# Kernel optimization log

Hardware: AMD Instinct MI355X
Metric: run time of the kernel (lower is better)

Reference implementation:

```python
import jax, jax.numpy as jnp
import numpy as np

N_NODES = 100000
N_EDGES = 1600000
IN_DIM, HID_DIM, OUT_DIM = 128, 64, 1


def setup_inputs() -> dict:
    key = jax.random.key(0)
    ks = jax.random.split(key, 8)
    x = jax.random.normal(ks[0], (N_NODES, IN_DIM), dtype=jnp.float32)
    edge_index = jax.random.randint(ks[1], (2, N_EDGES), 0, N_NODES, dtype=jnp.int64)
    # Glorot-ish scaled weights
    W1 = jax.random.normal(ks[2], (IN_DIM, HID_DIM), dtype=jnp.float32) / np.sqrt(IN_DIM)
    b1 = jnp.zeros((HID_DIM,), dtype=jnp.float32)
    W2 = jax.random.normal(ks[3], (HID_DIM, HID_DIM), dtype=jnp.float32) / np.sqrt(HID_DIM)
    b2 = jnp.zeros((HID_DIM,), dtype=jnp.float32)
    W3 = jax.random.normal(ks[4], (HID_DIM, OUT_DIM), dtype=jnp.float32) / np.sqrt(HID_DIM)
    b3 = jnp.zeros((OUT_DIM,), dtype=jnp.float32)
    return {"x": x, "edge_index": edge_index, "W1": W1, "b1": b1,
            "W2": W2, "b2": b2, "W3": W3, "b3": b3}


def _gcn_norm(edge_index, num_nodes):
    # PyG gcn_norm with add_self_loops=True, edge_weight=1:
    # deg[i] = 1 (self loop) + #incoming edges at i (dst = edge_index[1])
    dst = edge_index[1]
    deg = jnp.ones((num_nodes,), dtype=jnp.float32).at[dst].add(1.0)
    dis = jnp.where(deg > 0, 1.0 / jnp.sqrt(deg), 0.0)  # deg_inv_sqrt
    return dis


def _gcn_conv(x, W, b, src, dst, dis):
    h = x @ W                                   # [N, F_out] transform first (PyG order)
    norm = dis[src] * dis[dst]                  # [E]
    msg = h[src] * norm[:, None]                # gather + scale, [E, F_out]
    out = jnp.zeros_like(h).at[dst].add(msg)    # scatter-add aggregation
    out = out + h * (dis * dis)[:, None]        # self-loop contribution
    return out + b


def reference(x, edge_index, W1, b1, W2, b2, W3, b3):
    src, dst = edge_index[0], edge_index[1]
    dis = _gcn_norm(edge_index, x.shape[0])
    h = jax.nn.relu(_gcn_conv(x, W1, b1, src, dst, dis))   # dropout = identity (eval)
    h = jax.nn.relu(_gcn_conv(h, W2, b2, src, dst, dis))
    return _gcn_conv(h, W3, b3, src, dst, dis)
```

## Files before the change

### kernel.cpp

```cpp
#include <hip/hip_runtime.h>

#define IN_DIM 128
#define HID 64
#define MAXC 400
#define MAXB 512
#define EPB 4096
#define DPT 512
#define G1CAP 6144

static __device__ __forceinline__ unsigned short f2bf(float f) {
    unsigned u = __float_as_uint(f);
    u += 0x7FFF + ((u >> 16) & 1);
    return (unsigned short)(u >> 16);
}

typedef short bf16x8 __attribute__((ext_vector_type(8)));
typedef float f32x4 __attribute__((ext_vector_type(4)));

__global__ __launch_bounds__(256) void k_hist2(const int* __restrict__ dst,
                                               int* __restrict__ hmat, int E, int NC) {
    __shared__ int h[MAXC];
    int tid = threadIdx.x, blk = blockIdx.x;
    for (int i = tid; i < NC; i += 256) h[i] = 0;
    __syncthreads();
    int e0 = blk * EPB, e1 = min(e0 + EPB, E);
    for (int e = e0 + tid; e < e1; e += 256) atomicAdd(&h[dst[e] >> 8], 1);
    __syncthreads();
    for (int i = tid; i < NC; i += 256) hmat[blk * MAXC + i] = h[i];
}

__global__ __launch_bounds__(512) void k_bktscan(int* __restrict__ hmat,
                                                 int* __restrict__ bktTotal,
                                                 int NBLK, int NC) {
    __shared__ int tmp[512];
    int cb = blockIdx.x;
    int t = threadIdx.x;
    int v = (t < NBLK) ? hmat[t * MAXC + cb] : 0;
    tmp[t] = v;
    __syncthreads();
    for (int off = 1; off < 512; off <<= 1) {
        int a = (t >= off) ? tmp[t - off] : 0;
        __syncthreads();
        tmp[t] += a;
        __syncthreads();
    }
    if (t < NBLK) hmat[t * MAXC + cb] = tmp[t] - v;
    if (t == 511) bktTotal[cb] = tmp[511];
}

__global__ __launch_bounds__(512) void k_cscan(const int* __restrict__ bktTotal,
                                               int* __restrict__ coarseStart,
                                               int* __restrict__ rowStart,
                                               int NC, int N, int E) {
    __shared__ int tmp[512];
    int t = threadIdx.x;
    int v = (t < NC) ? bktTotal[t] : 0;
    tmp[t] = v;
    __syncthreads();
    for (int off = 1; off < 512; off <<= 1) {
        int a = (t >= off) ? tmp[t - off] : 0;
        __syncthreads();
        tmp[t] += a;
        __syncthreads();
    }
    int excl = tmp[t] - v;
    if (t < NC) coarseStart[t] = excl;
    if (t == NC - 1) coarseStart[NC] = excl + v;
    if (t == 0) rowStart[N] = E;
}

__global__ __launch_bounds__(256) void k_part1(const int* __restrict__ src,
                                               const int* __restrict__ dst,
                                               const int* __restrict__ hmat,
                                               const int* __restrict__ coarseStart,
                                               int* __restrict__ tmp1,
                                               int E, int NC) {
    __shared__ int bcnt[MAXC];
    __shared__ int bbase[MAXC];
    int tid = threadIdx.x, blk = blockIdx.x;
    for (int i = tid; i < NC; i += 256) {
        bcnt[i] = 0;
        bbase[i] = coarseStart[i] + hmat[blk * MAXC + i];
    }
    __syncthreads();
    int e0 = blk * EPB, e1 = min(e0 + EPB, E);
    for (int e = e0 + tid; e < e1; e += 256) {
        int s = src[e], d = dst[e];
        int cb = d >> 8;
        int slot = bbase[cb] + atomicAdd(&bcnt[cb], 1);
        tmp1[slot] = s | ((d & 255) << 17);
    }
}

__global__ __launch_bounds__(DPT) void k_degplace(const int* __restrict__ tmp1,
                                                  const int* __restrict__ coarseStart,
                                                  float* __restrict__ dis,
                                                  int* __restrict__ rowStart,
                                                  int* __restrict__ esrc, int N) {
    __shared__ int hist[256];
    __shared__ int scn[256];
    __shared__ int cur[256];
    int tid = threadIdx.x;
    int cb = blockIdx.x;
    int node0 = cb << 8;
    const int r0 = coarseStart[cb], r1 = coarseStart[cb + 1];
    if (tid < 256) hist[tid] = 0;
    __syncthreads();
    for (int i = r0 + tid; i < r1; i += DPT)
        atomicAdd(&hist[((unsigned)tmp1[i]) >> 17], 1);
    __syncthreads();
    int v = 0;
    if (tid < 256) { v = hist[tid]; scn[tid] = v; }
    __syncthreads();
    for (int off = 1; off < 256; off <<= 1) {
        int a = 0;
        if (tid < 256 && tid >= off) a = scn[tid - off];
        __syncthreads();
        if (tid < 256) scn[tid] += a;
        __syncthreads();
    }
    if (tid < 256) {
        int myStart = r0 + scn[tid] - v;
        cur[tid] = myStart;
        int node = node0 + tid;
        if (node < N) {
            dis[node] = rsqrtf((float)v + 1.0f);
            rowStart[node] = myStart;
        }
    }
    __syncthreads();
    for (int i = r0 + tid; i < r1; i += DPT) {
        int pk = tmp1[i];
        int dl = ((unsigned)pk) >> 17;
        int pos = atomicAdd(&cur[dl], 1);
        esrc[pos] = (pk & 0x1FFFF) << 7;
    }
}

template <int K, typename T>
__global__ __launch_bounds__(256) void k_mmx(const T* __restrict__ X,
                                             const float* __restrict__ W,
                                             const float* __restrict__ dis,
                                             unsigned short* __restrict__ Hbs, int N) {
    constexpr int WP = K + 8;
    __shared__ unsigned short Wt[64 * WP];
    const int tid = threadIdx.x;
    for (int i = tid; i < K * 64; i += 256) {
        int k = i >> 6, n = i & 63;
        Wt[n * WP + k] = f2bf(W[i]);
    }
    __syncthreads();
    const int lane = tid & 63;
    const int m16 = lane & 15;
    const int quad = lane >> 4;
    const int rowBase = blockIdx.x * 64 + (tid >> 6) * 16;
    const int rowc = min(rowBase + m16, N - 1);

    f32x4 acc0 = {0.f, 0.f, 0.f, 0.f};
    f32x4 acc1 = acc0, acc2 = acc0, acc3 = acc0;
    const T* xrow = X + (size_t)rowc * K;
#pragma unroll
    for (int k0 = 0; k0 < K; k0 += 32) {
        bf16x8 af;
        if constexpr (sizeof(T) == 4) {
            const float* xp = (const float*)xrow + k0 + quad * 8;
            float4 xa = *(const float4*)xp;
            float4 xb = *(const float4*)(xp + 4);
            af[0] = (short)f2bf(xa.x); af[1] = (short)f2bf(xa.y);
            af[2] = (short)f2bf(xa.z); af[3] = (short)f2bf(xa.w);
            af[4] = (short)f2bf(xb.x); af[5] = (short)f2bf(xb.y);
            af[6] = (short)f2bf(xb.z); af[7] = (short)f2bf(xb.w);
        } else {
            af = *(const bf16x8*)((const unsigned short*)xrow + k0 + quad * 8);
        }
        const unsigned short* wp = &Wt[m16 * WP + k0 + quad * 8];
        bf16x8 b0 = *(const bf16x8*)(wp);
        bf16x8 b1 = *(const bf16x8*)(wp + 16 * WP);
        bf16x8 b2 = *(const bf16x8*)(wp + 32 * WP);
        bf16x8 b3 = *(const bf16x8*)(wp + 48 * WP);
        acc0 = __builtin_amdgcn_mfma_f32_16x16x32_bf16(af, b0, acc0, 0, 0, 0);
        acc1 = __builtin_amdgcn_mfma_f32_16x16x32_bf16(af, b1, acc1, 0, 0, 0);
        acc2 = __builtin_amdgcn_mfma_f32_16x16x32_bf16(af, b2, acc2, 0, 0, 0);
        acc3 = __builtin_amdgcn_mfma_f32_16x16x32_bf16(af, b3, acc3, 0, 0, 0);
    }
#pragma unroll
    for (int reg = 0; reg < 4; ++reg) {
        int r = rowBase + quad * 4 + reg;
        if (r < N) {
            float dsc = dis[r];
            unsigned short* hp = Hbs + (size_t)r * 64 + m16;
            hp[0]  = f2bf(acc0[reg] * dsc);
            hp[16] = f2bf(acc1[reg] * dsc);
            hp[32] = f2bf(acc2[reg] * dsc);
            hp[48] = f2bf(acc3[reg] * dsc);
        }
    }
}


#define BLO(d) __uint_as_float((d) << 16)
#define BHI(d) __uint_as_float((d) & 0xFFFF0000u)
#define ACC2(A, Q) { A.x += BLO((Q).x); A.y += BHI((Q).x);                     \
                     A.z += BLO((Q).y); A.w += BHI((Q).y); }

template <int MODE>
__global__ __launch_bounds__(256) void k_gather64(const unsigned short* __restrict__ Hbs,
                                                  const int* __restrict__ esrc,
                                                  const int* __restrict__ rowStart,
                                                  const float* __restrict__ dis,
                                                  const float* __restrict__ b,
                                                  unsigned short* __restrict__ outB,
                                                  const float* __restrict__ W3,
                                                  const float* __restrict__ b3,
                                                  float* __restrict__ colS,
                                                  float* __restrict__ outF,
                                                  int N) {
    int lane = threadIdx.x & 63;
    int c = lane & 15;
    int sub = lane >> 4;
    int qb = sub << 4;
    int wave = (blockIdx.x * 256 + threadIdx.x) >> 6;
    int g0 = wave * 4;
    if (g0 >= N) return;
    const char* hb = (const char*)Hbs + c * 8;

    int rb = rowStart[min(g0 + lane, N)];
    int Rq  = __shfl(rb, sub, 64);
    int Rq1 = __shfl(rb, sub + 1, 64);
    int n = g0 + sub;
    int nc = min(n, N - 1);

    float4 a;
    {
        uint2 sd = *(const uint2*)(hb + ((size_t)nc << 7));
        a.x = BLO(sd.x); a.y = BHI(sd.x); a.z = BLO(sd.y); a.w = BHI(sd.y);
    }

    unsigned eoff = (Rq + c < Rq1) ? (unsigned)esrc[Rq + c] : 0u;
    for (int bb = Rq; bb < Rq1; bb += 16) {
        int cnt = min(16, Rq1 - bb);
        unsigned eoffN = (bb + 16 + c < Rq1) ? (unsigned)esrc[bb + 16 + c] : 0u;

        int j = 0;
        for (; j + 8 <= cnt; j += 8) {
            unsigned o0 = __shfl(eoff, qb + j + 0, 64);
            unsigned o1 = __shfl(eoff, qb + j + 1, 64);
            unsigned o2 = __shfl(eoff, qb + j + 2, 64);
            unsigned o3 = __shfl(eoff, qb + j + 3, 64);
            unsigned o4 = __shfl(eoff, qb + j + 4, 64);
            unsigned o5 = __shfl(eoff, qb + j + 5, 64);
            unsigned o6 = __shfl(eoff, qb + j + 6, 64);
            unsigned o7 = __shfl(eoff, qb + j + 7, 64);
            uint2 q0 = *(const uint2*)(hb + o0);
            uint2 q1 = *(const uint2*)(hb + o1);
            uint2 q2 = *(const uint2*)(hb + o2);
            uint2 q3 = *(const uint2*)(hb + o3);
            uint2 q4 = *(const uint2*)(hb + o4);
            uint2 q5 = *(const uint2*)(hb + o5);
            uint2 q6 = *(const uint2*)(hb + o6);
            uint2 q7 = *(const uint2*)(hb + o7);
            ACC2(a, q0) ACC2(a, q1) ACC2(a, q2) ACC2(a, q3)
            ACC2(a, q4) ACC2(a, q5) ACC2(a, q6) ACC2(a, q7)
        }
        if (j + 4 <= cnt) {
            unsigned o0 = __shfl(eoff, qb + j + 0, 64);
            unsigned o1 = __shfl(eoff, qb + j + 1, 64);
            unsigned o2 = __shfl(eoff, qb + j + 2, 64);
            unsigned o3 = __shfl(eoff, qb + j + 3, 64);
            uint2 q0 = *(const uint2*)(hb + o0);
            uint2 q1 = *(const uint2*)(hb + o1);
            uint2 q2 = *(const uint2*)(hb + o2);
            uint2 q3 = *(const uint2*)(hb + o3);
            ACC2(a, q0) ACC2(a, q1) ACC2(a, q2) ACC2(a, q3)
            j += 4;
        }
        if (j < cnt) {
            bool v1 = j + 1 < cnt, v2 = j + 2 < cnt;
            unsigned o0 = __shfl(eoff, qb + j, 64);
            unsigned o1 = __shfl(eoff, v1 ? qb + j + 1 : qb + j, 64);
            unsigned o2 = __shfl(eoff, v2 ? qb + j + 2 : qb + j, 64);
            uint2 q0 = *(const uint2*)(hb + o0);
            uint2 q1 = *(const uint2*)(hb + o1);
            uint2 q2 = *(const uint2*)(hb + o2);
            if (!v1) { q1.x = 0u; q1.y = 0u; }
            if (!v2) { q2.x = 0u; q2.y = 0u; }
            ACC2(a, q0) ACC2(a, q1) ACC2(a, q2)
        }
        eoff = eoffN;
    }

    float ds = dis[nc];
    float4 bl = ((const float4*)b)[c];
    float4 v;
    v.x = fmaxf(a.x * ds + bl.x, 0.f);
    v.y = fmaxf(a.y * ds + bl.y, 0.f);
    v.z = fmaxf(a.z * ds + bl.z, 0.f);
    v.w = fmaxf(a.w * ds + bl.w, 0.f);

    if (MODE == 1) {
        uint2 pv;
        pv.x = (unsigned)f2bf(v.x) | ((unsigned)f2bf(v.y) << 16);
        pv.y = (unsigned)f2bf(v.z) | ((unsigned)f2bf(v.w) << 16);
        if (n < N) ((uint2*)outB)[(size_t)n * 16 + c] = pv;
    } else {
        float4 w3 = ((const float4*)W3)[c];
        float t = v.x * w3.x + v.y * w3.y + v.z * w3.z + v.w * w3.w;
        t += __shfl_xor(t, 1, 64);
        t += __shfl_xor(t, 2, 64);
        t += __shfl_xor(t, 4, 64);
        t += __shfl_xor(t, 8, 64);
        if (c == 0 && n < N) {
            colS[n] = t * ds;
            outF[n] = t * ds * ds + b3[0];
        }
    }
}

__global__ __launch_bounds__(256) void k_gather1(const float* __restrict__ colS,
                                                 const int* __restrict__ esrc,
                                                 const int* __restrict__ rowStart,
                                                 const float* __restrict__ dis,
                                                 float* __restrict__ out, int N) {
    __shared__ float ls[G1CAP];
    int tid = threadIdx.x;
    int n0 = blockIdx.x * 256;
    int nEnd = min(n0 + 256, N);
    int r0 = rowStart[n0];
    int r1 = rowStart[nEnd];
    int cnt = r1 - r0;
    if (cnt <= G1CAP) {
        for (int i = tid; i < cnt; i += 256)
            ls[i] = colS[((unsigned)esrc[r0 + i]) >> 7];
        __syncthreads();
        int n = n0 + tid;
        if (n < N) {
            int a = rowStart[n] - r0, bnd = rowStart[n + 1] - r0;
            float acc = 0.0f;
            for (int e = a; e < bnd; ++e) acc += ls[e];
            out[n] += acc * dis[n];
        }
    } else {
        int n = n0 + tid;
        if (n < N) {
            int a = rowStart[n], bnd = rowStart[n + 1];
            float acc = 0.0f;
            for (int e = a; e < bnd; ++e) acc += colS[((unsigned)esrc[e]) >> 7];
            out[n] += acc * dis[n];
        }
    }
}

extern "C" void kernel_launch(void* const* d_in, const int* in_sizes, int n_in,
                              void* d_out, int out_size, void* d_ws, size_t ws_size,
                              hipStream_t stream) {
    const float* x  = (const float*)d_in[0];
    const int*   ei = (const int*)d_in[1];
    const float* W1 = (const float*)d_in[2];
    const float* b1 = (const float*)d_in[3];
    const float* W2 = (const float*)d_in[4];
    const float* b2 = (const float*)d_in[5];
    const float* W3 = (const float*)d_in[6];
    const float* b3 = (const float*)d_in[7];
    float* out = (float*)d_out;

    const int N = in_sizes[0] / IN_DIM;
    const int E = in_sizes[1] / 2;
    const int* src = ei;
    const int* dst = ei + E;
    const int NC = (N + 255) >> 8;
    const int NBLK = (E + EPB - 1) / EPB;

    char* w = (char*)d_ws;
    auto alloc = [&](size_t bytes) {
        char* p = w;
        w += (bytes + 1023) & ~(size_t)1023;
        return p;
    };
    float*          dis        = (float*)alloc((size_t)N * 4);
    unsigned short* Hbs        = (unsigned short*)alloc((size_t)N * 64 * 2);
    unsigned short* Hb1        = (unsigned short*)alloc((size_t)N * 64 * 2);
    float*          colS       = (float*)alloc((size_t)N * 4);
    int*            rowStart   = (int*)alloc((size_t)(N + 1) * 4);
    int*            bktTotal   = (int*)alloc((size_t)MAXC * 4);
    int*            coarseStart= (int*)alloc((size_t)(MAXC + 1) * 4);
    int*            hmat       = (int*)alloc((size_t)MAXB * MAXC * 4);
    int*            esrc       = (int*)alloc((size_t)E * 4);
    int*            tmp1       = (int*)alloc((size_t)E * 4);

    const int NB_N  = (N + 255) / 256;
    const int NB_MX = (N + 63) / 64;
    const int NB_G4 = ((N + 3) / 4 * 64 + 255) / 256;

    k_hist2<<<NBLK, 256, 0, stream>>>(dst, hmat, E, NC);
    k_bktscan<<<NC, 512, 0, stream>>>(hmat, bktTotal, NBLK, NC);
    k_cscan<<<1, 512, 0, stream>>>(bktTotal, coarseStart, rowStart, NC, N, E);
    k_part1<<<NBLK, 256, 0, stream>>>(src, dst, hmat, coarseStart, tmp1, E, NC);
    k_degplace<<<NC, DPT, 0, stream>>>(tmp1, coarseStart, dis, rowStart, esrc, N);

    k_mmx<IN_DIM, float><<<NB_MX, 256, 0, stream>>>(x, W1, dis, Hbs, N);
    k_gather64<1><<<NB_G4, 256, 0, stream>>>(Hbs, esrc, rowStart, dis, b1,
                                             Hb1, nullptr, nullptr, nullptr, nullptr, N);

    k_mmx<HID, unsigned short><<<NB_MX, 256, 0, stream>>>(Hb1, W2, dis, Hbs, N);
    k_gather64<2><<<NB_G4, 256, 0, stream>>>(Hbs, esrc, rowStart, dis, b2,
                                             nullptr, W3, b3, colS, out, N);

    k_gather1<<<NB_N, 256, 0, stream>>>(colS, esrc, rowStart, dis, out, N);
}
```

Baseline: 233.3 us.

## Replace two-level bucket CSR build with global-atomic degree count and scatter

Replaces the coarse-bucket partition plus per-bucket local sort CSR construction with a direct scheme. Per-node degrees come from global atomics, followed by a three-kernel prefix scan and an atomic-slot scatter of source offsets. This drops the tmp1 intermediate pass and the large hmat histogram, at the cost of contended global atomics and a non-deterministic edge order within rows. It also adds a fully unrolled 16-edge fast path in the gather loop to raise memory-level parallelism for full chunks.

```diff
diff --git a/kernel.cpp b/kernel.cpp
--- a/kernel.cpp
+++ b/kernel.cpp
@@ -2,10 +2,6 @@
 
 #define IN_DIM 128
 #define HID 64
-#define MAXC 400
-#define MAXB 512
-#define EPB 4096
-#define DPT 512
 #define G1CAP 6144
 
 static __device__ __forceinline__ unsigned short f2bf(float f) {
@@ -17,25 +13,52 @@
 typedef short bf16x8 __attribute__((ext_vector_type(8)));
 typedef float f32x4 __attribute__((ext_vector_type(4)));
 
-__global__ __launch_bounds__(256) void k_hist2(const int* __restrict__ dst,
-                                               int* __restrict__ hmat, int E, int NC) {
-    __shared__ int h[MAXC];
-    int tid = threadIdx.x, blk = blockIdx.x;
-    for (int i = tid; i < NC; i += 256) h[i] = 0;
+
+__global__ __launch_bounds__(256) void k_zero(int* __restrict__ deg, int N) {
+    int i = blockIdx.x * 256 + threadIdx.x;
+    if (i < N) deg[i] = 0;
+}
+
+__global__ __launch_bounds__(256) void k_deg(const int* __restrict__ dst,
+                                             int* __restrict__ deg, int E) {
+    int e = (blockIdx.x * 256 + threadIdx.x) * 4;
+    if (e + 4 <= E) {
+        int4 d = *(const int4*)(dst + e);
+        atomicAdd(&deg[d.x], 1);
+        atomicAdd(&deg[d.y], 1);
+        atomicAdd(&deg[d.z], 1);
+        atomicAdd(&deg[d.w], 1);
+    } else {
+        for (; e < E; ++e) atomicAdd(&deg[dst[e]], 1);
+    }
+}
+
+__global__ __launch_bounds__(256) void k_scanA(const int* __restrict__ deg,
+                                               int* __restrict__ rowStart,
+                                               int* __restrict__ blkSum, int N) {
+    __shared__ int tmp[256];
+    int i = blockIdx.x * 256 + threadIdx.x;
+    int t = threadIdx.x;
+    int v = (i < N) ? deg[i] : 0;
+    tmp[t] = v;
     __syncthreads();
-    int e0 = blk * EPB, e1 = min(e0 + EPB, E);
-    for (int e = e0 + tid; e < e1; e += 256) atomicAdd(&h[dst[e] >> 8], 1);
-    __syncthreads();
-    for (int i = tid; i < NC; i += 256) hmat[blk * MAXC + i] = h[i];
-}
-
-__global__ __launch_bounds__(512) void k_bktscan(int* __restrict__ hmat,
-                                                 int* __restrict__ bktTotal,
-                                                 int NBLK, int NC) {
+    for (int off = 1; off < 256; off <<= 1) {
+        int a = (t >= off) ? tmp[t - off] : 0;
+        __syncthreads();
+        tmp[t] += a;
+        __syncthreads();
+    }
+    if (i < N) rowStart[i] = tmp[t] - v;
+    if (t == 255) blkSum[blockIdx.x] = tmp[255];
+}
+
+__global__ __launch_bounds__(512) void k_scanB(const int* __restrict__ blkSum,
+                                               int* __restrict__ blkBase,
+                                               int NB, int* __restrict__ rowStart,
+                                               int N, int E) {
     __shared__ int tmp[512];
-    int cb = blockIdx.x;
     int t = threadIdx.x;
-    int v = (t < NBLK) ? hmat[t * MAXC + cb] : 0;
+    int v = (t < NB) ? blkSum[t] : 0;
     tmp[t] = v;
     __syncthreads();
     for (int off = 1; off < 512; off <<= 1) {
@@ -44,96 +67,41 @@
         tmp[t] += a;
         __syncthreads();
     }
-    if (t < NBLK) hmat[t * MAXC + cb] = tmp[t] - v;
-    if (t == 511) bktTotal[cb] = tmp[511];
-}
-
-__global__ __launch_bounds__(512) void k_cscan(const int* __restrict__ bktTotal,
-                                               int* __restrict__ coarseStart,
+    if (t < NB) blkBase[t] = tmp[t] - v;
+    if (t == 0) rowStart[N] = E;
+}
+
+__global__ __launch_bounds__(256) void k_scanC(const int* __restrict__ blkBase,
+                                               const int* __restrict__ deg,
                                                int* __restrict__ rowStart,
-                                               int NC, int N, int E) {
-    __shared__ int tmp[512];
-    int t = threadIdx.x;
-    int v = (t < NC) ? bktTotal[t] : 0;
-    tmp[t] = v;
-    __syncthreads();
-    for (int off = 1; off < 512; off <<= 1) {
-        int a = (t >= off) ? tmp[t - off] : 0;
-        __syncthreads();
-        tmp[t] += a;
-        __syncthreads();
-    }
-    int excl = tmp[t] - v;
-    if (t < NC) coarseStart[t] = excl;
-    if (t == NC - 1) coarseStart[NC] = excl + v;
-    if (t == 0) rowStart[N] = E;
-}
-
-__global__ __launch_bounds__(256) void k_part1(const int* __restrict__ src,
+                                               int* __restrict__ cur,
+                                               float* __restrict__ dis, int N) {
+    int i = blockIdx.x * 256 + threadIdx.x;
+    if (i < N) {
+        int r = rowStart[i] + blkBase[blockIdx.x];
+        rowStart[i] = r;
+        cur[i] = r;
+        dis[i] = rsqrtf((float)deg[i] + 1.0f);
+    }
+}
+
+__global__ __launch_bounds__(256) void k_place(const int* __restrict__ src,
                                                const int* __restrict__ dst,
-                                               const int* __restrict__ hmat,
-                                               const int* __restrict__ coarseStart,
-                                               int* __restrict__ tmp1,
-                                               int E, int NC) {
-    __shared__ int bcnt[MAXC];
-    __shared__ int bbase[MAXC];
-    int tid = threadIdx.x, blk = blockIdx.x;
-    for (int i = tid; i < NC; i += 256) {
-        bcnt[i] = 0;
-        bbase[i] = coarseStart[i] + hmat[blk * MAXC + i];
-    }
-    __syncthreads();
-    int e0 = blk * EPB, e1 = min(e0 + EPB, E);
-    for (int e = e0 + tid; e < e1; e += 256) {
-        int s = src[e], d = dst[e];
-        int cb = d >> 8;
-        int slot = bbase[cb] + atomicAdd(&bcnt[cb], 1);
-        tmp1[slot] = s | ((d & 255) << 17);
-    }
-}
-
-__global__ __launch_bounds__(DPT) void k_degplace(const int* __restrict__ tmp1,
-                                                  const int* __restrict__ coarseStart,
-                                                  float* __restrict__ dis,
-                                                  int* __restrict__ rowStart,
-                                                  int* __restrict__ esrc, int N) {
-    __shared__ int hist[256];
-    __shared__ int scn[256];
-    __shared__ int cur[256];
-    int tid = threadIdx.x;
-    int cb = blockIdx.x;
-    int node0 = cb << 8;
-    const int r0 = coarseStart[cb], r1 = coarseStart[cb + 1];
-    if (tid < 256) hist[tid] = 0;
-    __syncthreads();
-    for (int i = r0 + tid; i < r1; i += DPT)
-        atomicAdd(&hist[((unsigned)tmp1[i]) >> 17], 1);
-    __syncthreads();
-    int v = 0;
-    if (tid < 256) { v = hist[tid]; scn[tid] = v; }
-    __syncthreads();
-    for (int off = 1; off < 256; off <<= 1) {
-        int a = 0;
-        if (tid < 256 && tid >= off) a = scn[tid - off];
-        __syncthreads();
-        if (tid < 256) scn[tid] += a;
-        __syncthreads();
-    }
-    if (tid < 256) {
-        int myStart = r0 + scn[tid] - v;
-        cur[tid] = myStart;
-        int node = node0 + tid;
-        if (node < N) {
-            dis[node] = rsqrtf((float)v + 1.0f);
-            rowStart[node] = myStart;
-        }
-    }
-    __syncthreads();
-    for (int i = r0 + tid; i < r1; i += DPT) {
-        int pk = tmp1[i];
-        int dl = ((unsigned)pk) >> 17;
-        int pos = atomicAdd(&cur[dl], 1);
-        esrc[pos] = (pk & 0x1FFFF) << 7;
+                                               int* __restrict__ cur,
+                                               int* __restrict__ esrc, int E) {
+    int e = (blockIdx.x * 256 + threadIdx.x) * 4;
+    if (e + 4 <= E) {
+        int4 s = *(const int4*)(src + e);
+        int4 d = *(const int4*)(dst + e);
+        int p0 = atomicAdd(&cur[d.x], 1); esrc[p0] = s.x << 7;
+        int p1 = atomicAdd(&cur[d.y], 1); esrc[p1] = s.y << 7;
+        int p2 = atomicAdd(&cur[d.z], 1); esrc[p2] = s.z << 7;
+        int p3 = atomicAdd(&cur[d.w], 1); esrc[p3] = s.w << 7;
+    } else {
+        for (; e < E; ++e) {
+            int p = atomicAdd(&cur[dst[e]], 1);
+            esrc[p] = src[e] << 7;
+        }
     }
 }
 
@@ -242,15 +210,23 @@
         unsigned eoffN = (bb + 16 + c < Rq1) ? (unsigned)esrc[bb + 16 + c] : 0u;
 
         int j = 0;
-        for (; j + 8 <= cnt; j += 8) {
-            unsigned o0 = __shfl(eoff, qb + j + 0, 64);
-            unsigned o1 = __shfl(eoff, qb + j + 1, 64);
-            unsigned o2 = __shfl(eoff, qb + j + 2, 64);
-            unsigned o3 = __shfl(eoff, qb + j + 3, 64);
-            unsigned o4 = __shfl(eoff, qb + j + 4, 64);
-            unsigned o5 = __shfl(eoff, qb + j + 5, 64);
-            unsigned o6 = __shfl(eoff, qb + j + 6, 64);
-            unsigned o7 = __shfl(eoff, qb + j + 7, 64);
+        if (cnt == 16) {
+            unsigned o0 = __shfl(eoff, qb + 0, 64);
+            unsigned o1 = __shfl(eoff, qb + 1, 64);
+            unsigned o2 = __shfl(eoff, qb + 2, 64);
+            unsigned o3 = __shfl(eoff, qb + 3, 64);
+            unsigned o4 = __shfl(eoff, qb + 4, 64);
+            unsigned o5 = __shfl(eoff, qb + 5, 64);
+            unsigned o6 = __shfl(eoff, qb + 6, 64);
+            unsigned o7 = __shfl(eoff, qb + 7, 64);
+            unsigned o8 = __shfl(eoff, qb + 8, 64);
+            unsigned o9 = __shfl(eoff, qb + 9, 64);
+            unsigned oA = __shfl(eoff, qb + 10, 64);
+            unsigned oB = __shfl(eoff, qb + 11, 64);
+            unsigned oC = __shfl(eoff, qb + 12, 64);
+            unsigned oD = __shfl(eoff, qb + 13, 64);
+            unsigned oE = __shfl(eoff, qb + 14, 64);
+            unsigned oF = __shfl(eoff, qb + 15, 64);
             uint2 q0 = *(const uint2*)(hb + o0);
             uint2 q1 = *(const uint2*)(hb + o1);
             uint2 q2 = *(const uint2*)(hb + o2);
@@ -259,32 +235,64 @@
             uint2 q5 = *(const uint2*)(hb + o5);
             uint2 q6 = *(const uint2*)(hb + o6);
             uint2 q7 = *(const uint2*)(hb + o7);
+            uint2 q8 = *(const uint2*)(hb + o8);
+            uint2 q9 = *(const uint2*)(hb + o9);
+            uint2 qA = *(const uint2*)(hb + oA);
+            uint2 qB = *(const uint2*)(hb + oB);
+            uint2 qC = *(const uint2*)(hb + oC);
+            uint2 qD = *(const uint2*)(hb + oD);
+            uint2 qE = *(const uint2*)(hb + oE);
+            uint2 qF = *(const uint2*)(hb + oF);
             ACC2(a, q0) ACC2(a, q1) ACC2(a, q2) ACC2(a, q3)
             ACC2(a, q4) ACC2(a, q5) ACC2(a, q6) ACC2(a, q7)
-        }
-        if (j + 4 <= cnt) {
-            unsigned o0 = __shfl(eoff, qb + j + 0, 64);
-            unsigned o1 = __shfl(eoff, qb + j + 1, 64);
-            unsigned o2 = __shfl(eoff, qb + j + 2, 64);
-            unsigned o3 = __shfl(eoff, qb + j + 3, 64);
-            uint2 q0 = *(const uint2*)(hb + o0);
-            uint2 q1 = *(const uint2*)(hb + o1);
-            uint2 q2 = *(const uint2*)(hb + o2);
-            uint2 q3 = *(const uint2*)(hb + o3);
-            ACC2(a, q0) ACC2(a, q1) ACC2(a, q2) ACC2(a, q3)
-            j += 4;
-        }
-        if (j < cnt) {
-            bool v1 = j + 1 < cnt, v2 = j + 2 < cnt;
-            unsigned o0 = __shfl(eoff, qb + j, 64);
-            unsigned o1 = __shfl(eoff, v1 ? qb + j + 1 : qb + j, 64);
-            unsigned o2 = __shfl(eoff, v2 ? qb + j + 2 : qb + j, 64);
-            uint2 q0 = *(const uint2*)(hb + o0);
-            uint2 q1 = *(const uint2*)(hb + o1);
-            uint2 q2 = *(const uint2*)(hb + o2);
-            if (!v1) { q1.x = 0u; q1.y = 0u; }
-            if (!v2) { q2.x = 0u; q2.y = 0u; }
-            ACC2(a, q0) ACC2(a, q1) ACC2(a, q2)
+            ACC2(a, q8) ACC2(a, q9) ACC2(a, qA) ACC2(a, qB)
+            ACC2(a, qC) ACC2(a, qD) ACC2(a, qE) ACC2(a, qF)
+            j = 16;
+        } else {
+            for (; j + 8 <= cnt; j += 8) {
+                unsigned o0 = __shfl(eoff, qb + j + 0, 64);
+                unsigned o1 = __shfl(eoff, qb + j + 1, 64);
+                unsigned o2 = __shfl(eoff, qb + j + 2, 64);
+                unsigned o3 = __shfl(eoff, qb + j + 3, 64);
+                unsigned o4 = __shfl(eoff, qb + j + 4, 64);
+                unsigned o5 = __shfl(eoff, qb + j + 5, 64);
+                unsigned o6 = __shfl(eoff, qb + j + 6, 64);
+                unsigned o7 = __shfl(eoff, qb + j + 7, 64);
+                uint2 q0 = *(const uint2*)(hb + o0);
+                uint2 q1 = *(const uint2*)(hb + o1);
+                uint2 q2 = *(const uint2*)(hb + o2);
+                uint2 q3 = *(const uint2*)(hb + o3);
+                uint2 q4 = *(const uint2*)(hb + o4);
+                uint2 q5 = *(const uint2*)(hb + o5);
+                uint2 q6 = *(const uint2*)(hb + o6);
+                uint2 q7 = *(const uint2*)(hb + o7);
+                ACC2(a, q0) ACC2(a, q1) ACC2(a, q2) ACC2(a, q3)
+                ACC2(a, q4) ACC2(a, q5) ACC2(a, q6) ACC2(a, q7)
+            }
+            if (j + 4 <= cnt) {
+                unsigned o0 = __shfl(eoff, qb + j + 0, 64);
+                unsigned o1 = __shfl(eoff, qb + j + 1, 64);
+                unsigned o2 = __shfl(eoff, qb + j + 2, 64);
+                unsigned o3 = __shfl(eoff, qb + j + 3, 64);
+                uint2 q0 = *(const uint2*)(hb + o0);
+                uint2 q1 = *(const uint2*)(hb + o1);
+                uint2 q2 = *(const uint2*)(hb + o2);
+                uint2 q3 = *(const uint2*)(hb + o3);
+                ACC2(a, q0) ACC2(a, q1) ACC2(a, q2) ACC2(a, q3)
+                j += 4;
+            }
+            if (j < cnt) {
+                bool v1 = j + 1 < cnt, v2 = j + 2 < cnt;
+                unsigned o0 = __shfl(eoff, qb + j, 64);
+                unsigned o1 = __shfl(eoff, v1 ? qb + j + 1 : qb + j, 64);
+                unsigned o2 = __shfl(eoff, v2 ? qb + j + 2 : qb + j, 64);
+                uint2 q0 = *(const uint2*)(hb + o0);
+                uint2 q1 = *(const uint2*)(hb + o1);
+                uint2 q2 = *(const uint2*)(hb + o2);
+                if (!v1) { q1.x = 0u; q1.y = 0u; }
+                if (!v2) { q2.x = 0u; q2.y = 0u; }
+                ACC2(a, q0) ACC2(a, q1) ACC2(a, q2)
+            }
         }
         eoff = eoffN;
     }
@@ -367,8 +375,6 @@
     const int E = in_sizes[1] / 2;
     const int* src = ei;
     const int* dst = ei + E;
-    const int NC = (N + 255) >> 8;
-    const int NBLK = (E + EPB - 1) / EPB;
 
     char* w = (char*)d_ws;
     auto alloc = [&](size_t bytes) {
@@ -381,21 +387,23 @@
     unsigned short* Hb1        = (unsigned short*)alloc((size_t)N * 64 * 2);
     float*          colS       = (float*)alloc((size_t)N * 4);
     int*            rowStart   = (int*)alloc((size_t)(N + 1) * 4);
-    int*            bktTotal   = (int*)alloc((size_t)MAXC * 4);
-    int*            coarseStart= (int*)alloc((size_t)(MAXC + 1) * 4);
-    int*            hmat       = (int*)alloc((size_t)MAXB * MAXC * 4);
+    int*            deg        = (int*)alloc((size_t)N * 4);
+    int*            cur        = (int*)alloc((size_t)N * 4);
+    int*            blkSum     = (int*)alloc((size_t)512 * 4);
+    int*            blkBase    = (int*)alloc((size_t)512 * 4);
     int*            esrc       = (int*)alloc((size_t)E * 4);
-    int*            tmp1       = (int*)alloc((size_t)E * 4);
 
     const int NB_N  = (N + 255) / 256;
+    const int NB_E4 = ((E + 3) / 4 + 255) / 256;
     const int NB_MX = (N + 63) / 64;
     const int NB_G4 = ((N + 3) / 4 * 64 + 255) / 256;
 
-    k_hist2<<<NBLK, 256, 0, stream>>>(dst, hmat, E, NC);
-    k_bktscan<<<NC, 512, 0, stream>>>(hmat, bktTotal, NBLK, NC);
-    k_cscan<<<1, 512, 0, stream>>>(bktTotal, coarseStart, rowStart, NC, N, E);
-    k_part1<<<NBLK, 256, 0, stream>>>(src, dst, hmat, coarseStart, tmp1, E, NC);
-    k_degplace<<<NC, DPT, 0, stream>>>(tmp1, coarseStart, dis, rowStart, esrc, N);
+    k_zero <<<NB_N,  256, 0, stream>>>(deg, N);
+    k_deg  <<<NB_E4, 256, 0, stream>>>(dst, deg, E);
+    k_scanA<<<NB_N,  256, 0, stream>>>(deg, rowStart, blkSum, N);
+    k_scanB<<<1,     512, 0, stream>>>(blkSum, blkBase, NB_N, rowStart, N, E);
+    k_scanC<<<NB_N,  256, 0, stream>>>(blkBase, deg, rowStart, cur, dis, N);
+    k_place<<<NB_E4, 256, 0, stream>>>(src, dst, cur, esrc, E);
 
     k_mmx<IN_DIM, float><<<NB_MX, 256, 0, stream>>>(x, W1, dis, Hbs, N);
     k_gather64<1><<<NB_G4, 256, 0, stream>>>(Hbs, esrc, rowStart, dis, b1,
```

Result: slower. 401.6 us (+72.2%).

## Fuse CSR partition kernels into one cooperative kernel with grid syncs

Applied to the files above, without the earlier changes.

Replaces the five separate partitioning launches (histogram, bucket scan, coarse scan, partition, degree/placement) with a single cooperative kernel that separates phases with grid.sync(). The aim is to remove four kernel launch gaps and the tail drain between them. It keeps the old multi-kernel path as a fallback if the cooperative launch fails. Grid syncs have their own cost, and the kernel uses 512-thread blocks for the histogram phases where the old kernels used 256.

```diff
diff --git a/kernel.cpp b/kernel.cpp
--- a/kernel.cpp
+++ b/kernel.cpp
@@ -1,4 +1,7 @@
 #include <hip/hip_runtime.h>
+#include <hip/hip_cooperative_groups.h>
+
+namespace cg = cooperative_groups;
 
 #define IN_DIM 128
 #define HID 64
@@ -16,6 +19,117 @@
 
 typedef short bf16x8 __attribute__((ext_vector_type(8)));
 typedef float f32x4 __attribute__((ext_vector_type(4)));
+
+__global__ __launch_bounds__(512) void k_partition(
+    const int* __restrict__ src, const int* __restrict__ dst,
+    int* __restrict__ hmat, int* __restrict__ bktTotal,
+    int* __restrict__ coarseStart, float* __restrict__ dis,
+    int* __restrict__ rowStart, int* __restrict__ esrc,
+    int* __restrict__ tmp1, int N, int E, int NC, int NBLK)
+{
+    cg::grid_group grid = cg::this_grid();
+    __shared__ int sA[MAXC];
+    __shared__ int sB[MAXC];
+    __shared__ int sc[512];
+    const int tid = threadIdx.x;
+    const int blk = blockIdx.x;
+
+    if (blk < NBLK) {
+        for (int i = tid; i < NC; i += 512) sA[i] = 0;
+        __syncthreads();
+        int e0 = blk * EPB, e1 = min(e0 + EPB, E);
+        for (int e = e0 + tid; e < e1; e += 512) atomicAdd(&sA[dst[e] >> 8], 1);
+        __syncthreads();
+        for (int i = tid; i < NC; i += 512) hmat[blk * MAXC + i] = sA[i];
+    }
+    grid.sync();
+
+    if (blk < NC) {
+        int cb = blk;
+        int v = (tid < NBLK) ? hmat[tid * MAXC + cb] : 0;
+        sc[tid] = v;
+        __syncthreads();
+        for (int off = 1; off < 512; off <<= 1) {
+            int a = (tid >= off) ? sc[tid - off] : 0;
+            __syncthreads();
+            sc[tid] += a;
+            __syncthreads();
+        }
+        if (tid < NBLK) hmat[tid * MAXC + cb] = sc[tid] - v;
+        if (tid == 511) bktTotal[cb] = sc[511];
+    }
+    grid.sync();
+
+    if (blk == 0) {
+        int v = (tid < NC) ? bktTotal[tid] : 0;
+        sc[tid] = v;
+        __syncthreads();
+        for (int off = 1; off < 512; off <<= 1) {
+            int a = (tid >= off) ? sc[tid - off] : 0;
+            __syncthreads();
+            sc[tid] += a;
+            __syncthreads();
+        }
+        int excl = sc[tid] - v;
+        if (tid < NC) coarseStart[tid] = excl;
+        if (tid == NC - 1) coarseStart[NC] = excl + v;
+        if (tid == 0) rowStart[N] = E;
+    }
+    grid.sync();
+
+    if (blk < NBLK) {
+        for (int i = tid; i < NC; i += 512) {
+            sA[i] = 0;
+            sB[i] = coarseStart[i] + hmat[blk * MAXC + i];
+        }
+        __syncthreads();
+        int e0 = blk * EPB, e1 = min(e0 + EPB, E);
+        for (int e = e0 + tid; e < e1; e += 512) {
+            int s = src[e], d = dst[e];
+            int cb = d >> 8;
+            int slot = sB[cb] + atomicAdd(&sA[cb], 1);
+            tmp1[slot] = s | ((d & 255) << 17);
+        }
+    }
+    grid.sync();
+
+    if (blk < NC) {
+        int cb = blk;
+        int node0 = cb << 8;
+        const int r0 = coarseStart[cb], r1 = coarseStart[cb + 1];
+        if (tid < 256) sA[tid] = 0;
+        __syncthreads();
+        for (int i = r0 + tid; i < r1; i += 512)
+            atomicAdd(&sA[((unsigned)tmp1[i]) >> 17], 1);
+        __syncthreads();
+        int v = 0;
+        if (tid < 256) { v = sA[tid]; sc[tid] = v; }
+        __syncthreads();
+        for (int off = 1; off < 256; off <<= 1) {
+            int a = 0;
+            if (tid < 256 && tid >= off) a = sc[tid - off];
+            __syncthreads();
+            if (tid < 256) sc[tid] += a;
+            __syncthreads();
+        }
+        if (tid < 256) {
+            int myStart = r0 + sc[tid] - v;
+            sB[tid] = myStart;
+            int node = node0 + tid;
+            if (node < N) {
+                dis[node] = rsqrtf((float)v + 1.0f);
+                rowStart[node] = myStart;
+            }
+        }
+        __syncthreads();
+        for (int i = r0 + tid; i < r1; i += 512) {
+            int pk = tmp1[i];
+            int dl = ((unsigned)pk) >> 17;
+            int pos = atomicAdd(&sB[dl], 1);
+            esrc[pos] = (pk & 0x1FFFF) << 7;
+        }
+    }
+}
 
 __global__ __launch_bounds__(256) void k_hist2(const int* __restrict__ dst,
                                                int* __restrict__ hmat, int E, int NC) {
@@ -363,12 +477,12 @@
     const float* b3 = (const float*)d_in[7];
     float* out = (float*)d_out;
 
-    const int N = in_sizes[0] / IN_DIM;
-    const int E = in_sizes[1] / 2;
+    int N = in_sizes[0] / IN_DIM;
+    int E = in_sizes[1] / 2;
     const int* src = ei;
     const int* dst = ei + E;
-    const int NC = (N + 255) >> 8;
-    const int NBLK = (E + EPB - 1) / EPB;
+    int NC = (N + 255) >> 8;
+    int NBLK = (E + EPB - 1) / EPB;
 
     char* w = (char*)d_ws;
     auto alloc = [&](size_t bytes) {
@@ -390,12 +504,25 @@
     const int NB_N  = (N + 255) / 256;
     const int NB_MX = (N + 63) / 64;
     const int NB_G4 = ((N + 3) / 4 * 64 + 255) / 256;
-
-    k_hist2<<<NBLK, 256, 0, stream>>>(dst, hmat, E, NC);
-    k_bktscan<<<NC, 512, 0, stream>>>(hmat, bktTotal, NBLK, NC);
-    k_cscan<<<1, 512, 0, stream>>>(bktTotal, coarseStart, rowStart, NC, N, E);
-    k_part1<<<NBLK, 256, 0, stream>>>(src, dst, hmat, coarseStart, tmp1, E, NC);
-    k_degplace<<<NC, DPT, 0, stream>>>(tmp1, coarseStart, dis, rowStart, esrc, N);
+    const int GP = (NBLK > NC) ? NBLK : NC;
+
+    {
+        void* args[] = {(void*)&src, (void*)&dst, (void*)&hmat, (void*)&bktTotal,
+                        (void*)&coarseStart, (void*)&dis, (void*)&rowStart,
+                        (void*)&esrc, (void*)&tmp1, (void*)&N, (void*)&E,
+                        (void*)&NC, (void*)&NBLK};
+        hipError_t cerr = hipLaunchCooperativeKernel((void*)k_partition,
+                                                     dim3(GP), dim3(512),
+                                                     args, 0, stream);
+        if (cerr != hipSuccess) {
+            (void)hipGetLastError();
+            k_hist2<<<NBLK, 256, 0, stream>>>(dst, hmat, E, NC);
+            k_bktscan<<<NC, 512, 0, stream>>>(hmat, bktTotal, NBLK, NC);
+            k_cscan<<<1, 512, 0, stream>>>(bktTotal, coarseStart, rowStart, NC, N, E);
+            k_part1<<<NBLK, 256, 0, stream>>>(src, dst, hmat, coarseStart, tmp1, E, NC);
+            k_degplace<<<NC, DPT, 0, stream>>>(tmp1, coarseStart, dis, rowStart, esrc, N);
+        }
+    }
 
     k_mmx<IN_DIM, float><<<NB_MX, 256, 0, stream>>>(x, W1, dis, Hbs, N);
     k_gather64<1><<<NB_G4, 256, 0, stream>>>(Hbs, esrc, rowStart, dis, b1,
```

After: 446.2 us. 1.91x slower.
